# Performance work log

Hardware: AMD Instinct MI355X
Metric: run time of the kernel (lower is better)

Reference implementation:

```python
import jax, jax.numpy as jnp
import numpy as np

N, E = 50000, 800000
DIN, DH, DOUT = 128, 128, 64


def _w(k, fan_in, fan_out):
    return (jax.random.normal(k, (fan_in, fan_out), jnp.float32) / np.sqrt(fan_in)).astype(jnp.float32)


def setup_inputs() -> dict:
    key = jax.random.key(0)
    ks = jax.random.split(key, 12)
    x = jax.random.normal(ks[0], (N, DIN), jnp.float32)
    edge_index = jax.random.randint(ks[1], (2, E), 0, N, dtype=jnp.int64)
    return {
        "x": x,
        "edge_index": edge_index,
        # sage1 block: SAGEConv(DIN->DH) -> relu -> SAGEConv(DH->DH)
        "Ws11": _w(ks[2], DIN, DH), "Wn11": _w(ks[3], DIN, DH), "b11": jnp.zeros((DH,), jnp.float32),
        "Ws12": _w(ks[4], DH, DH),  "Wn12": _w(ks[5], DH, DH),  "b12": jnp.zeros((DH,), jnp.float32),
        # sage2 block: SAGEConv(DH->DH) -> relu -> SAGEConv(DH->DH)
        "Ws21": _w(ks[6], DH, DH),  "Wn21": _w(ks[7], DH, DH),  "b21": jnp.zeros((DH,), jnp.float32),
        "Ws22": _w(ks[8], DH, DH),  "Wn22": _w(ks[9], DH, DH),  "b22": jnp.zeros((DH,), jnp.float32),
        # classifier
        "Wc": _w(ks[10], DH, DOUT), "bc": jnp.zeros((DOUT,), jnp.float32),
    }


def _sage_conv(h, src, tgt, Ws, Wn, b, n):
    # mean-aggregate neighbor features (src -> tgt), then self + neighbor linear
    msgs = h[src]                                                   # [E, d] gather
    deg = jax.ops.segment_sum(jnp.ones((src.shape[0],), h.dtype), tgt, num_segments=n)
    agg = jax.ops.segment_sum(msgs, tgt, num_segments=n)
    agg = agg / jnp.maximum(deg, 1.0)[:, None]                      # [n, d]
    return h @ Ws + agg @ Wn + b


def reference(x, edge_index, Ws11, Wn11, b11, Ws12, Wn12, b12,
              Ws21, Wn21, b21, Ws22, Wn22, b22, Wc, bc):
    src, tgt = edge_index[0], edge_index[1]
    n = x.shape[0]
    # sage1 block (2 layers) + outer relu
    h = jax.nn.relu(_sage_conv(x, src, tgt, Ws11, Wn11, b11, n))
    h = _sage_conv(h, src, tgt, Ws12, Wn12, b12, n)
    h = jax.nn.relu(h)
    # dropout (eval mode): identity
    # sage2 block (2 layers) + outer relu
    h = jax.nn.relu(_sage_conv(h, src, tgt, Ws21, Wn21, b21, n))
    h = _sage_conv(h, src, tgt, Ws22, Wn22, b22, n)
    h = jax.nn.relu(h)
    # global mean pool over nodes, then classify
    g = jnp.mean(h, axis=0)                                         # [DH]
    return g @ Wc + bc                                              # [DOUT]
```

## Files before the change

### kernel.cpp

```cpp
#include <hip/hip_runtime.h>
#include <hip/hip_bf16.h>
#include <hip/hip_fp16.h>


typedef _Float16 f16x8 __attribute__((ext_vector_type(8)));
typedef float f32x4 __attribute__((ext_vector_type(4)));

__global__ __launch_bounds__(256) void k_bucket(
    const int* __restrict__ src, const int* __restrict__ tgt,
    int* __restrict__ deg, unsigned long long* __restrict__ staging,
    int* __restrict__ bucket_fill, int E, int bdiv, int cap) {
  __shared__ unsigned long long buf[8][320];
  __shared__ int cnt[8];
  __shared__ int base[8];
  int tid = threadIdx.x;
  int lane = tid & 63;
  if (tid < 8) cnt[tid] = 0;
  __syncthreads();
  int e0 = blockIdx.x * 2048;
#pragma unroll
  for (int i = 0; i < 8; ++i) {
    int e = e0 + i * 256 + tid;
    int b = -1;
    unsigned long long pair = 0;
    if (e < E) {
      int t = tgt[e];
      int s = src[e];
      atomicAdd(&deg[t], 1);
      b = t / bdiv;
      pair = ((unsigned long long)(unsigned)t << 32) | (unsigned)s;
    }
#pragma unroll
    for (int bk = 0; bk < 8; ++bk) {
      bool mine = (b == bk);
      unsigned long long mask = __ballot(mine);
      if (mask == 0ull) continue;
      int cw = __popcll(mask);
      int leader = __ffsll((unsigned long long)mask) - 1;
      int p0 = 0;
      if (lane == leader) p0 = atomicAdd(&cnt[bk], cw);
      p0 = __shfl(p0, leader, 64);
      if (mine) {
        int p = p0 + __popcll(mask & ((1ull << lane) - 1ull));
        if (p < 320) {
          buf[bk][p] = pair;
        } else {
          int gp = atomicAdd(&bucket_fill[bk], 1);
          staging[(size_t)bk * cap + gp] = pair;
        }
      }
    }
  }
  __syncthreads();
  if (tid < 8) {
    int c = min(cnt[tid], 320);
    base[tid] = atomicAdd(&bucket_fill[tid], c);
    cnt[tid] = c;
  }
  __syncthreads();
  for (int b = 0; b < 8; ++b) {
    int c = cnt[b];
    for (int p = tid; p < c; p += 256)
      staging[(size_t)b * cap + base[b] + p] = buf[b][p];
  }
}

__global__ __launch_bounds__(256) void k_scatter2(
    const unsigned long long* __restrict__ staging,
    const int* __restrict__ bucket_fill, int* __restrict__ cursor,
    int* __restrict__ csr_src, int cap) {
  int b = blockIdx.x & 7;
  int nchunk = gridDim.x >> 3;
  int chunk = blockIdx.x >> 3;
  int n = bucket_fill[b];
  const unsigned long long* sb = staging + (size_t)b * cap;
  for (int i0 = chunk * 2048; i0 < n; i0 += nchunk * 2048) {
#pragma unroll
    for (int t = 0; t < 8; ++t) {
      int i = i0 + t * 256 + (int)threadIdx.x;
      if (i < n) {
        unsigned long long pair = sb[i];
        int tg = (int)(pair >> 32);
        int s = (int)(pair & 0xffffffffu);
        int pos = atomicAdd(&cursor[tg], 1);
        csr_src[pos] = s;
      }
    }
  }
}

__global__ __launch_bounds__(256) void k_scan1(const int* __restrict__ deg,
                                               int* __restrict__ partial,
                                               int* __restrict__ blocksum,
                                               float* __restrict__ inv_deg, int n) {
  __shared__ int s[256];
  int tid = threadIdx.x;
  int i = blockIdx.x * 256 + tid;
  int v = (i < n) ? deg[i] : 0;
  s[tid] = v;
  __syncthreads();
  for (int off = 1; off < 256; off <<= 1) {
    int t = (tid >= off) ? s[tid - off] : 0;
    __syncthreads();
    s[tid] += t;
    __syncthreads();
  }
  if (i < n) {
    partial[i] = s[tid] - v;
    inv_deg[i] = 1.0f / fmaxf((float)v, 1.0f);
  }
  if (tid == 255) blocksum[blockIdx.x] = s[255];
}

__global__ __launch_bounds__(256) void k_scan2(int* __restrict__ blocksum, int nb) {
  __shared__ int s[256];
  int tid = threadIdx.x;
  int v = (tid < nb) ? blocksum[tid] : 0;
  s[tid] = v;
  __syncthreads();
  for (int off = 1; off < 256; off <<= 1) {
    int t = (tid >= off) ? s[tid - off] : 0;
    __syncthreads();
    s[tid] += t;
    __syncthreads();
  }
  if (tid < nb) blocksum[tid] = s[tid] - v;
}

__global__ __launch_bounds__(256) void k_scan3(const int* __restrict__ partial,
                                               const int* __restrict__ blocksum,
                                               int* __restrict__ row_start,
                                               int* __restrict__ cursor, int n, int E) {
  int i = blockIdx.x * 256 + threadIdx.x;
  if (i < n) {
    int r = partial[i] + blocksum[blockIdx.x];
    row_start[i] = r;
    cursor[i] = r;
  }
  if (i == 0) row_start[n] = E;
}

__global__ __launch_bounds__(256) void k_cvt_x(const float* __restrict__ x,
                                               __half* __restrict__ xh, int total8) {
  int i = blockIdx.x * 256 + threadIdx.x;
  if (i >= total8) return;
  const float4* p = (const float4*)(x + (size_t)i * 8);
  float4 v0 = p[0], v1 = p[1];
  f16x8 o;
  o[0] = (_Float16)v0.x; o[1] = (_Float16)v0.y; o[2] = (_Float16)v0.z; o[3] = (_Float16)v0.w;
  o[4] = (_Float16)v1.x; o[5] = (_Float16)v1.y; o[6] = (_Float16)v1.z; o[7] = (_Float16)v1.w;
  *(f16x8*)(xh + (size_t)i * 8) = o;
}

struct WPack {
  const float* s[4];
  const float* n[4];
};

__global__ __launch_bounds__(256) void k_prep_w(WPack p, __half* __restrict__ Wt) {
  int l = blockIdx.y;
  int i = blockIdx.x * 256 + threadIdx.x;
  int n = i >> 8;
  int k = i & 255;
  const float* W = (k < 128) ? p.s[l] : p.n[l];
  float v = W[(size_t)(k & 127) * 128 + n];
  Wt[(size_t)l * 32768 + (size_t)n * 256 + k] = __float2half(v);
}

__global__ __launch_bounds__(256) void k_agg_h(
    const __half* __restrict__ h, const int* __restrict__ csr_src,
    const int* __restrict__ row_start, const float* __restrict__ inv_deg,
    __half* __restrict__ agg, int n_nodes) {
  int gw = (blockIdx.x * 256 + (int)threadIdx.x) >> 6;
  int lane = threadIdx.x & 63;
  if (gw >= n_nodes) return;
  int q = lane >> 4;
  int dl = (lane & 15) * 8;
  int beg = row_start[gw];
  int end = row_start[gw + 1];
  float a0 = 0.f, a1 = 0.f, a2 = 0.f, a3 = 0.f;
  float a4 = 0.f, a5 = 0.f, a6 = 0.f, a7 = 0.f;
  int e = beg;
  for (; e + 16 <= end; e += 16) {
    int i0 = csr_src[e + q];
    int i1 = csr_src[e + 4 + q];
    int i2 = csr_src[e + 8 + q];
    int i3 = csr_src[e + 12 + q];
    f16x8 v0 = *(const f16x8*)(h + (size_t)i0 * 128 + dl);
    f16x8 v1 = *(const f16x8*)(h + (size_t)i1 * 128 + dl);
    f16x8 v2 = *(const f16x8*)(h + (size_t)i2 * 128 + dl);
    f16x8 v3 = *(const f16x8*)(h + (size_t)i3 * 128 + dl);
    a0 += ((float)v0[0] + (float)v1[0]) + ((float)v2[0] + (float)v3[0]);
    a1 += ((float)v0[1] + (float)v1[1]) + ((float)v2[1] + (float)v3[1]);
    a2 += ((float)v0[2] + (float)v1[2]) + ((float)v2[2] + (float)v3[2]);
    a3 += ((float)v0[3] + (float)v1[3]) + ((float)v2[3] + (float)v3[3]);
    a4 += ((float)v0[4] + (float)v1[4]) + ((float)v2[4] + (float)v3[4]);
    a5 += ((float)v0[5] + (float)v1[5]) + ((float)v2[5] + (float)v3[5]);
    a6 += ((float)v0[6] + (float)v1[6]) + ((float)v2[6] + (float)v3[6]);
    a7 += ((float)v0[7] + (float)v1[7]) + ((float)v2[7] + (float)v3[7]);
  }
  for (; e + 8 <= end; e += 8) {
    int i0 = csr_src[e + q];
    int i1 = csr_src[e + 4 + q];
    f16x8 v0 = *(const f16x8*)(h + (size_t)i0 * 128 + dl);
    f16x8 v1 = *(const f16x8*)(h + (size_t)i1 * 128 + dl);
    a0 += (float)v0[0] + (float)v1[0];
    a1 += (float)v0[1] + (float)v1[1];
    a2 += (float)v0[2] + (float)v1[2];
    a3 += (float)v0[3] + (float)v1[3];
    a4 += (float)v0[4] + (float)v1[4];
    a5 += (float)v0[5] + (float)v1[5];
    a6 += (float)v0[6] + (float)v1[6];
    a7 += (float)v0[7] + (float)v1[7];
  }
  for (; e + 4 <= end; e += 4) {
    int i0 = csr_src[e + q];
    f16x8 v0 = *(const f16x8*)(h + (size_t)i0 * 128 + dl);
    a0 += (float)v0[0];
    a1 += (float)v0[1];
    a2 += (float)v0[2];
    a3 += (float)v0[3];
    a4 += (float)v0[4];
    a5 += (float)v0[5];
    a6 += (float)v0[6];
    a7 += (float)v0[7];
  }
  if (e + q < end) {
    int i0 = csr_src[e + q];
    f16x8 v0 = *(const f16x8*)(h + (size_t)i0 * 128 + dl);
    a0 += (float)v0[0];
    a1 += (float)v0[1];
    a2 += (float)v0[2];
    a3 += (float)v0[3];
    a4 += (float)v0[4];
    a5 += (float)v0[5];
    a6 += (float)v0[6];
    a7 += (float)v0[7];
  }
  a0 += __shfl_xor(a0, 16, 64);
  a1 += __shfl_xor(a1, 16, 64);
  a2 += __shfl_xor(a2, 16, 64);
  a3 += __shfl_xor(a3, 16, 64);
  a4 += __shfl_xor(a4, 16, 64);
  a5 += __shfl_xor(a5, 16, 64);
  a6 += __shfl_xor(a6, 16, 64);
  a7 += __shfl_xor(a7, 16, 64);
  a0 += __shfl_xor(a0, 32, 64);
  a1 += __shfl_xor(a1, 32, 64);
  a2 += __shfl_xor(a2, 32, 64);
  a3 += __shfl_xor(a3, 32, 64);
  a4 += __shfl_xor(a4, 32, 64);
  a5 += __shfl_xor(a5, 32, 64);
  a6 += __shfl_xor(a6, 32, 64);
  a7 += __shfl_xor(a7, 32, 64);
  if (q == 0) {
    float wgt = inv_deg[gw];
    f16x8 r;
    r[0] = (_Float16)(a0 * wgt);
    r[1] = (_Float16)(a1 * wgt);
    r[2] = (_Float16)(a2 * wgt);
    r[3] = (_Float16)(a3 * wgt);
    r[4] = (_Float16)(a4 * wgt);
    r[5] = (_Float16)(a5 * wgt);
    r[6] = (_Float16)(a6 * wgt);
    r[7] = (_Float16)(a7 * wgt);
    *(f16x8*)(agg + (size_t)gw * 128 + dl) = r;
  }
}

__global__ __launch_bounds__(256) void k_linear_mfma(
    const __half* __restrict__ h, const __half* __restrict__ agg,
    const __half* __restrict__ Wt, const float* __restrict__ bias,
    __half* __restrict__ out, int n_nodes) {
  int tid = threadIdx.x;
  int cq = tid >> 6;
  int lane = tid & 63;
  int node0 = blockIdx.x * 64;
  int lr = lane & 15;
  int lg = lane >> 4;

  f16x8 bs[8][2];
#pragma unroll
  for (int ks = 0; ks < 8; ++ks) {
    int kb = ks * 32 + lg * 8;
    bs[ks][0] = *(const f16x8*)(Wt + (size_t)(cq * 32 + lr) * 256 + kb);
    bs[ks][1] = *(const f16x8*)(Wt + (size_t)(cq * 32 + 16 + lr) * 256 + kb);
  }

  f32x4 acc[4][2];
#pragma unroll
  for (int rt = 0; rt < 4; ++rt)
#pragma unroll
    for (int ct = 0; ct < 2; ++ct) acc[rt][ct] = (f32x4){0.f, 0.f, 0.f, 0.f};

  const __half* hrow[4];
  const __half* grow[4];
#pragma unroll
  for (int rt = 0; rt < 4; ++rt) {
    int arow = node0 + rt * 16 + lr;
    if (arow >= n_nodes) arow = n_nodes - 1;
    hrow[rt] = h + (size_t)arow * 128;
    grow[rt] = agg + (size_t)arow * 128;
  }

#pragma unroll
  for (int ks = 0; ks < 8; ++ks) {
    int koff = (ks & 3) * 32 + lg * 8;
#pragma unroll
    for (int rt = 0; rt < 4; ++rt) {
      f16x8 a = (ks < 4) ? *(const f16x8*)(hrow[rt] + koff)
                         : *(const f16x8*)(grow[rt] + koff);
      acc[rt][0] = __builtin_amdgcn_mfma_f32_16x16x32_f16(a, bs[ks][0], acc[rt][0], 0, 0, 0);
      acc[rt][1] = __builtin_amdgcn_mfma_f32_16x16x32_f16(a, bs[ks][1], acc[rt][1], 0, 0, 0);
    }
  }

#pragma unroll
  for (int ct = 0; ct < 2; ++ct) {
    int n_col = cq * 32 + ct * 16 + lr;
    float bv = bias[n_col];
#pragma unroll
    for (int rt = 0; rt < 4; ++rt) {
#pragma unroll
      for (int r = 0; r < 4; ++r) {
        int m = node0 + rt * 16 + lg * 4 + r;
        if (m < n_nodes)
          out[(size_t)m * 128 + n_col] = __float2half(fmaxf(acc[rt][ct][r] + bv, 0.f));
      }
    }
  }
}

__global__ __launch_bounds__(256) void k_pool(const __half* __restrict__ h,
                                              float* __restrict__ partial, int n_nodes) {
  __shared__ float red[4][128];
  int tid = threadIdx.x;
  int lane = tid & 63;
  int w = tid >> 6;
  float a0 = 0.f, a1 = 0.f;
  for (int n = blockIdx.x * 4 + w; n < n_nodes; n += gridDim.x * 4) {
    float2 f = __half22float2(*(const __half2*)(h + (size_t)n * 128 + lane * 2));
    a0 += f.x;
    a1 += f.y;
  }
  red[w][lane * 2] = a0;
  red[w][lane * 2 + 1] = a1;
  __syncthreads();
  if (tid < 128) {
    partial[(size_t)blockIdx.x * 128 + tid] =
        (red[0][tid] + red[1][tid]) + (red[2][tid] + red[3][tid]);
  }
}

__global__ __launch_bounds__(512) void k_final(const float* __restrict__ partial,
                                               const float* __restrict__ Wc,
                                               const float* __restrict__ bc,
                                               float* __restrict__ out, int n_nodes) {
  __shared__ float red[4][128];
  __shared__ float gs[128];
  __shared__ float red2[8][64];
  int tid = threadIdx.x;
  int j = tid & 127;
  int c = tid >> 7;
  float s = 0.f;
#pragma unroll
  for (int b = 0; b < 64; ++b) s += partial[(size_t)(c * 64 + b) * 128 + j];
  red[c][j] = s;
  __syncthreads();
  if (tid < 128) {
    float g = (red[0][tid] + red[1][tid]) + (red[2][tid] + red[3][tid]);
    gs[tid] = g / (float)n_nodes;
  }
  __syncthreads();
  {
    int jo = tid & 63;
    int c2 = tid >> 6;
    float s2 = 0.f;
#pragma unroll
    for (int d = 0; d < 16; ++d)
      s2 += gs[c2 * 16 + d] * Wc[(size_t)(c2 * 16 + d) * 64 + jo];
    red2[c2][jo] = s2;
  }
  __syncthreads();
  if (tid < 64) {
    float o = bc[tid];
#pragma unroll
    for (int c2 = 0; c2 < 8; ++c2) o += red2[c2][tid];
    out[tid] = o;
  }
}

extern "C" void kernel_launch(void* const* d_in, const int* in_sizes, int n_in,
                              void* d_out, int out_size, void* d_ws, size_t ws_size,
                              hipStream_t stream) {
  const float* x = (const float*)d_in[0];
  const int* ei = (const int*)d_in[1];
  const float* Ws11 = (const float*)d_in[2];
  const float* Wn11 = (const float*)d_in[3];
  const float* b11 = (const float*)d_in[4];
  const float* Ws12 = (const float*)d_in[5];
  const float* Wn12 = (const float*)d_in[6];
  const float* b12 = (const float*)d_in[7];
  const float* Ws21 = (const float*)d_in[8];
  const float* Wn21 = (const float*)d_in[9];
  const float* b21 = (const float*)d_in[10];
  const float* Ws22 = (const float*)d_in[11];
  const float* Wn22 = (const float*)d_in[12];
  const float* b22 = (const float*)d_in[13];
  const float* Wc = (const float*)d_in[14];
  const float* bc = (const float*)d_in[15];

  int N = in_sizes[0] / 128;
  int E = in_sizes[1] / 2;
  const int* src = ei;
  const int* tgt = ei + E;

  int bdiv = (N + 7) / 8;
  int cap = E / 8 + 8192;

  char* w = (char*)d_ws;
  size_t off = 0;
  auto alloc = [&](size_t bytes) {
    void* p = w + off;
    off += (bytes + 255) & ~(size_t)255;
    return p;
  };
  __half* xh = (__half*)alloc((size_t)N * 128 * 2);
  __half* hA = (__half*)alloc((size_t)N * 128 * 2);
  __half* hB = (__half*)alloc((size_t)N * 128 * 2);
  __half* aggb = (__half*)alloc((size_t)N * 128 * 2);
  __half* Wt = (__half*)alloc((size_t)4 * 32768 * 2);
  float* partial = (float*)alloc((size_t)256 * 128 * 4);
  float* inv_deg = (float*)alloc((size_t)N * 4);
  int* deg = (int*)alloc((size_t)N * 4);
  int* row_start = (int*)alloc((size_t)(N + 1) * 4);
  int* cursor = (int*)alloc((size_t)N * 4);
  int* csr_src = (int*)alloc((size_t)E * 4);
  int* scanp = (int*)alloc((size_t)N * 4);
  int* blocksum = (int*)alloc((size_t)256 * 4);
  unsigned long long* staging =
      (unsigned long long*)alloc((size_t)8 * cap * 8);
  int* bucket_fill = (int*)alloc((size_t)8 * 4);

  hipMemsetAsync(deg, 0, (size_t)N * 4, stream);
  hipMemsetAsync(bucket_fill, 0, 8 * 4, stream);
  hipMemsetAsync(partial, 0, (size_t)256 * 128 * 4, stream);

  int nb = (N + 255) / 256;
  int bb = (E + 2047) / 2048;
  k_bucket<<<bb, 256, 0, stream>>>(src, tgt, deg, staging, bucket_fill, E, bdiv, cap);
  k_scan1<<<nb, 256, 0, stream>>>(deg, scanp, blocksum, inv_deg, N);
  k_scan2<<<1, 256, 0, stream>>>(blocksum, nb);
  k_scan3<<<nb, 256, 0, stream>>>(scanp, blocksum, row_start, cursor, N, E);
  k_scatter2<<<448, 256, 0, stream>>>(staging, bucket_fill, cursor, csr_src, cap);

  int total8 = N * 128 / 8;
  k_cvt_x<<<(total8 + 255) / 256, 256, 0, stream>>>(x, xh, total8);
  WPack wp;
  wp.s[0] = Ws11; wp.s[1] = Ws12; wp.s[2] = Ws21; wp.s[3] = Ws22;
  wp.n[0] = Wn11; wp.n[1] = Wn12; wp.n[2] = Wn21; wp.n[3] = Wn22;
  k_prep_w<<<dim3(128, 4), 256, 0, stream>>>(wp, Wt);

  int ab = (N + 3) / 4;
  int lb = (N + 63) / 64;

  k_agg_h<<<ab, 256, 0, stream>>>(xh, csr_src, row_start, inv_deg, aggb, N);
  k_linear_mfma<<<lb, 256, 0, stream>>>(xh, aggb, Wt + 0 * 32768, b11, hA, N);
  k_agg_h<<<ab, 256, 0, stream>>>(hA, csr_src, row_start, inv_deg, aggb, N);
  k_linear_mfma<<<lb, 256, 0, stream>>>(hA, aggb, Wt + 1 * 32768, b12, hB, N);
  k_agg_h<<<ab, 256, 0, stream>>>(hB, csr_src, row_start, inv_deg, aggb, N);
  k_linear_mfma<<<lb, 256, 0, stream>>>(hB, aggb, Wt + 2 * 32768, b21, hA, N);
  k_agg_h<<<ab, 256, 0, stream>>>(hA, csr_src, row_start, inv_deg, aggb, N);
  k_linear_mfma<<<lb, 256, 0, stream>>>(hA, aggb, Wt + 3 * 32768, b22, hB, N);

  k_pool<<<256, 256, 0, stream>>>(hB, partial, N);
  k_final<<<1, 512, 0, stream>>>(partial, Wc, bc, (float*)d_out, N);
}
```

Measured before the change: 349.4 us.

## Gather neighbor features as FP8 e4m3 with fp16 packed accumulation

Adds FP8 (e4m3) copies of the node features. The input conversion kernel writes one, and a new conversion kernel runs after each linear layer. The aggregation kernel now gathers these 8-bit rows, halving the bytes per random gather. Each FP8 value is expanded to fp16 by bit manipulation with a 256 scale fix, and sums are accumulated in packed half2 instead of fp32. This adds an extra conversion pass per layer and costs considerable accuracy, both from FP8 quantization and from fp16 accumulation over high-degree nodes.

Result: no change. 344.4 us (-1.4%).

```diff
diff --git a/kernel.cpp b/kernel.cpp
--- a/kernel.cpp
+++ b/kernel.cpp
@@ -1,6 +1,7 @@
 #include <hip/hip_runtime.h>
 #include <hip/hip_bf16.h>
 #include <hip/hip_fp16.h>
+#include <hip/hip_fp8.h>
 
 
 typedef _Float16 f16x8 __attribute__((ext_vector_type(8)));
@@ -141,15 +142,39 @@
 }
 
 __global__ __launch_bounds__(256) void k_cvt_x(const float* __restrict__ x,
-                                               __half* __restrict__ xh, int total8) {
+                                               __half* __restrict__ xh,
+                                               unsigned char* __restrict__ xh8,
+                                               int total8) {
   int i = blockIdx.x * 256 + threadIdx.x;
   if (i >= total8) return;
   const float4* p = (const float4*)(x + (size_t)i * 8);
   float4 v0 = p[0], v1 = p[1];
+  float f[8] = {v0.x, v0.y, v0.z, v0.w, v1.x, v1.y, v1.z, v1.w};
   f16x8 o;
-  o[0] = (_Float16)v0.x; o[1] = (_Float16)v0.y; o[2] = (_Float16)v0.z; o[3] = (_Float16)v0.w;
-  o[4] = (_Float16)v1.x; o[5] = (_Float16)v1.y; o[6] = (_Float16)v1.z; o[7] = (_Float16)v1.w;
+  unsigned long long u8 = 0;
+#pragma unroll
+  for (int j = 0; j < 8; ++j) {
+    o[j] = (_Float16)f[j];
+    __hip_fp8_e4m3 q(f[j]);
+    u8 |= (unsigned long long)(*reinterpret_cast<unsigned char*>(&q)) << (8 * j);
+  }
   *(f16x8*)(xh + (size_t)i * 8) = o;
+  *(unsigned long long*)(xh8 + (size_t)i * 8) = u8;
+}
+
+__global__ __launch_bounds__(256) void k_h8(const __half* __restrict__ h,
+                                            unsigned char* __restrict__ h8,
+                                            int total8) {
+  int i = blockIdx.x * 256 + threadIdx.x;
+  if (i >= total8) return;
+  f16x8 v = *(const f16x8*)(h + (size_t)i * 8);
+  unsigned long long u8 = 0;
+#pragma unroll
+  for (int j = 0; j < 8; ++j) {
+    __hip_fp8_e4m3 q((float)v[j]);
+    u8 |= (unsigned long long)(*reinterpret_cast<unsigned char*>(&q)) << (8 * j);
+  }
+  *(unsigned long long*)(h8 + (size_t)i * 8) = u8;
 }
 
 struct WPack {
@@ -167,8 +192,8 @@
   Wt[(size_t)l * 32768 + (size_t)n * 256 + k] = __float2half(v);
 }
 
-__global__ __launch_bounds__(256) void k_agg_h(
-    const __half* __restrict__ h, const int* __restrict__ csr_src,
+__global__ __launch_bounds__(256) void k_agg8(
+    const unsigned char* __restrict__ h8, const int* __restrict__ csr_src,
     const int* __restrict__ row_start, const float* __restrict__ inv_deg,
     __half* __restrict__ agg, int n_nodes) {
   int gw = (blockIdx.x * 256 + (int)threadIdx.x) >> 6;
@@ -178,92 +203,77 @@
   int dl = (lane & 15) * 8;
   int beg = row_start[gw];
   int end = row_start[gw + 1];
-  float a0 = 0.f, a1 = 0.f, a2 = 0.f, a3 = 0.f;
-  float a4 = 0.f, a5 = 0.f, a6 = 0.f, a7 = 0.f;
+  __half2 ac0 = __float2half2_rn(0.f), ac1 = ac0, ac2 = ac0, ac3 = ac0;
+
+  auto accum = [&](uint2 w) {
+    unsigned v0 = w.x, v1 = w.y;
+    unsigned e0 = ((v0 & 0x00800080u) << 8) | ((v0 & 0x007f007fu) << 7);
+    unsigned o0 = (((v0 >> 8) & 0x00800080u) << 8) | (((v0 >> 8) & 0x007f007fu) << 7);
+    unsigned e1 = ((v1 & 0x00800080u) << 8) | ((v1 & 0x007f007fu) << 7);
+    unsigned o1 = (((v1 >> 8) & 0x00800080u) << 8) | (((v1 >> 8) & 0x007f007fu) << 7);
+    ac0 = __hadd2(ac0, *reinterpret_cast<__half2*>(&e0));
+    ac1 = __hadd2(ac1, *reinterpret_cast<__half2*>(&o0));
+    ac2 = __hadd2(ac2, *reinterpret_cast<__half2*>(&e1));
+    ac3 = __hadd2(ac3, *reinterpret_cast<__half2*>(&o1));
+  };
+
   int e = beg;
   for (; e + 16 <= end; e += 16) {
     int i0 = csr_src[e + q];
     int i1 = csr_src[e + 4 + q];
     int i2 = csr_src[e + 8 + q];
     int i3 = csr_src[e + 12 + q];
-    f16x8 v0 = *(const f16x8*)(h + (size_t)i0 * 128 + dl);
-    f16x8 v1 = *(const f16x8*)(h + (size_t)i1 * 128 + dl);
-    f16x8 v2 = *(const f16x8*)(h + (size_t)i2 * 128 + dl);
-    f16x8 v3 = *(const f16x8*)(h + (size_t)i3 * 128 + dl);
-    a0 += ((float)v0[0] + (float)v1[0]) + ((float)v2[0] + (float)v3[0]);
-    a1 += ((float)v0[1] + (float)v1[1]) + ((float)v2[1] + (float)v3[1]);
-    a2 += ((float)v0[2] + (float)v1[2]) + ((float)v2[2] + (float)v3[2]);
-    a3 += ((float)v0[3] + (float)v1[3]) + ((float)v2[3] + (float)v3[3]);
-    a4 += ((float)v0[4] + (float)v1[4]) + ((float)v2[4] + (float)v3[4]);
-    a5 += ((float)v0[5] + (float)v1[5]) + ((float)v2[5] + (float)v3[5]);
-    a6 += ((float)v0[6] + (float)v1[6]) + ((float)v2[6] + (float)v3[6]);
-    a7 += ((float)v0[7] + (float)v1[7]) + ((float)v2[7] + (float)v3[7]);
+    uint2 w0 = *(const uint2*)(h8 + (size_t)i0 * 128 + dl);
+    uint2 w1 = *(const uint2*)(h8 + (size_t)i1 * 128 + dl);
+    uint2 w2 = *(const uint2*)(h8 + (size_t)i2 * 128 + dl);
+    uint2 w3 = *(const uint2*)(h8 + (size_t)i3 * 128 + dl);
+    accum(w0);
+    accum(w1);
+    accum(w2);
+    accum(w3);
   }
   for (; e + 8 <= end; e += 8) {
     int i0 = csr_src[e + q];
     int i1 = csr_src[e + 4 + q];
-    f16x8 v0 = *(const f16x8*)(h + (size_t)i0 * 128 + dl);
-    f16x8 v1 = *(const f16x8*)(h + (size_t)i1 * 128 + dl);
-    a0 += (float)v0[0] + (float)v1[0];
-    a1 += (float)v0[1] + (float)v1[1];
-    a2 += (float)v0[2] + (float)v1[2];
-    a3 += (float)v0[3] + (float)v1[3];
-    a4 += (float)v0[4] + (float)v1[4];
-    a5 += (float)v0[5] + (float)v1[5];
-    a6 += (float)v0[6] + (float)v1[6];
-    a7 += (float)v0[7] + (float)v1[7];
+    uint2 w0 = *(const uint2*)(h8 + (size_t)i0 * 128 + dl);
+    uint2 w1 = *(const uint2*)(h8 + (size_t)i1 * 128 + dl);
+    accum(w0);
+    accum(w1);
   }
   for (; e + 4 <= end; e += 4) {
     int i0 = csr_src[e + q];
-    f16x8 v0 = *(const f16x8*)(h + (size_t)i0 * 128 + dl);
-    a0 += (float)v0[0];
-    a1 += (float)v0[1];
-    a2 += (float)v0[2];
-    a3 += (float)v0[3];
-    a4 += (float)v0[4];
-    a5 += (float)v0[5];
-    a6 += (float)v0[6];
-    a7 += (float)v0[7];
+    accum(*(const uint2*)(h8 + (size_t)i0 * 128 + dl));
   }
   if (e + q < end) {
     int i0 = csr_src[e + q];
-    f16x8 v0 = *(const f16x8*)(h + (size_t)i0 * 128 + dl);
-    a0 += (float)v0[0];
-    a1 += (float)v0[1];
-    a2 += (float)v0[2];
-    a3 += (float)v0[3];
-    a4 += (float)v0[4];
-    a5 += (float)v0[5];
-    a6 += (float)v0[6];
-    a7 += (float)v0[7];
-  }
-  a0 += __shfl_xor(a0, 16, 64);
-  a1 += __shfl_xor(a1, 16, 64);
-  a2 += __shfl_xor(a2, 16, 64);
-  a3 += __shfl_xor(a3, 16, 64);
-  a4 += __shfl_xor(a4, 16, 64);
-  a5 += __shfl_xor(a5, 16, 64);
-  a6 += __shfl_xor(a6, 16, 64);
-  a7 += __shfl_xor(a7, 16, 64);
-  a0 += __shfl_xor(a0, 32, 64);
-  a1 += __shfl_xor(a1, 32, 64);
-  a2 += __shfl_xor(a2, 32, 64);
-  a3 += __shfl_xor(a3, 32, 64);
-  a4 += __shfl_xor(a4, 32, 64);
-  a5 += __shfl_xor(a5, 32, 64);
-  a6 += __shfl_xor(a6, 32, 64);
-  a7 += __shfl_xor(a7, 32, 64);
+    accum(*(const uint2*)(h8 + (size_t)i0 * 128 + dl));
+  }
+#pragma unroll
+  for (int off = 16; off <= 32; off <<= 1) {
+    int t0 = __shfl_xor(*reinterpret_cast<int*>(&ac0), off, 64);
+    int t1 = __shfl_xor(*reinterpret_cast<int*>(&ac1), off, 64);
+    int t2 = __shfl_xor(*reinterpret_cast<int*>(&ac2), off, 64);
+    int t3 = __shfl_xor(*reinterpret_cast<int*>(&ac3), off, 64);
+    ac0 = __hadd2(ac0, *reinterpret_cast<__half2*>(&t0));
+    ac1 = __hadd2(ac1, *reinterpret_cast<__half2*>(&t1));
+    ac2 = __hadd2(ac2, *reinterpret_cast<__half2*>(&t2));
+    ac3 = __hadd2(ac3, *reinterpret_cast<__half2*>(&t3));
+  }
   if (q == 0) {
-    float wgt = inv_deg[gw];
+    float wgt = inv_deg[gw] * 256.0f;
+    float2 f0 = __half22float2(ac0);
+    float2 f1 = __half22float2(ac1);
+    float2 f2 = __half22float2(ac2);
+    float2 f3 = __half22float2(ac3);
     f16x8 r;
-    r[0] = (_Float16)(a0 * wgt);
-    r[1] = (_Float16)(a1 * wgt);
-    r[2] = (_Float16)(a2 * wgt);
-    r[3] = (_Float16)(a3 * wgt);
-    r[4] = (_Float16)(a4 * wgt);
-    r[5] = (_Float16)(a5 * wgt);
-    r[6] = (_Float16)(a6 * wgt);
-    r[7] = (_Float16)(a7 * wgt);
+    r[0] = (_Float16)(f0.x * wgt);
+    r[1] = (_Float16)(f1.x * wgt);
+    r[2] = (_Float16)(f0.y * wgt);
+    r[3] = (_Float16)(f1.y * wgt);
+    r[4] = (_Float16)(f2.x * wgt);
+    r[5] = (_Float16)(f3.x * wgt);
+    r[6] = (_Float16)(f2.y * wgt);
+    r[7] = (_Float16)(f3.y * wgt);
     *(f16x8*)(agg + (size_t)gw * 128 + dl) = r;
   }
 }
@@ -429,6 +439,9 @@
   __half* hA = (__half*)alloc((size_t)N * 128 * 2);
   __half* hB = (__half*)alloc((size_t)N * 128 * 2);
   __half* aggb = (__half*)alloc((size_t)N * 128 * 2);
+  unsigned char* xh8 = (unsigned char*)alloc((size_t)N * 128);
+  unsigned char* h8A = (unsigned char*)alloc((size_t)N * 128);
+  unsigned char* h8B = (unsigned char*)alloc((size_t)N * 128);
   __half* Wt = (__half*)alloc((size_t)4 * 32768 * 2);
   float* partial = (float*)alloc((size_t)256 * 128 * 4);
   float* inv_deg = (float*)alloc((size_t)N * 4);
@@ -455,7 +468,8 @@
   k_scatter2<<<448, 256, 0, stream>>>(staging, bucket_fill, cursor, csr_src, cap);
 
   int total8 = N * 128 / 8;
-  k_cvt_x<<<(total8 + 255) / 256, 256, 0, stream>>>(x, xh, total8);
+  int cb = (total8 + 255) / 256;
+  k_cvt_x<<<cb, 256, 0, stream>>>(x, xh, xh8, total8);
   WPack wp;
   wp.s[0] = Ws11; wp.s[1] = Ws12; wp.s[2] = Ws21; wp.s[3] = Ws22;
   wp.n[0] = Wn11; wp.n[1] = Wn12; wp.n[2] = Wn21; wp.n[3] = Wn22;
@@ -464,13 +478,16 @@
   int ab = (N + 3) / 4;
   int lb = (N + 63) / 64;
 
-  k_agg_h<<<ab, 256, 0, stream>>>(xh, csr_src, row_start, inv_deg, aggb, N);
+  k_agg8<<<ab, 256, 0, stream>>>(xh8, csr_src, row_start, inv_deg, aggb, N);
   k_linear_mfma<<<lb, 256, 0, stream>>>(xh, aggb, Wt + 0 * 32768, b11, hA, N);
-  k_agg_h<<<ab, 256, 0, stream>>>(hA, csr_src, row_start, inv_deg, aggb, N);
+  k_h8<<<cb, 256, 0, stream>>>(hA, h8A, total8);
+  k_agg8<<<ab, 256, 0, stream>>>(h8A, csr_src, row_start, inv_deg, aggb, N);
   k_linear_mfma<<<lb, 256, 0, stream>>>(hA, aggb, Wt + 1 * 32768, b12, hB, N);
-  k_agg_h<<<ab, 256, 0, stream>>>(hB, csr_src, row_start, inv_deg, aggb, N);
+  k_h8<<<cb, 256, 0, stream>>>(hB, h8B, total8);
+  k_agg8<<<ab, 256, 0, stream>>>(h8B, csr_src, row_start, inv_deg, aggb, N);
   k_linear_mfma<<<lb, 256, 0, stream>>>(hB, aggb, Wt + 2 * 32768, b21, hA, N);
-  k_agg_h<<<ab, 256, 0, stream>>>(hA, csr_src, row_start, inv_deg, aggb, N);
+  k_h8<<<cb, 256, 0, stream>>>(hA, h8A, total8);
+  k_agg8<<<ab, 256, 0, stream>>>(h8A, csr_src, row_start, inv_deg, aggb, N);
   k_linear_mfma<<<lb, 256, 0, stream>>>(hA, aggb, Wt + 3 * 32768, b22, hB, N);
 
   k_pool<<<256, 256, 0, stream>>>(hB, partial, N);
```
